# Optimization experiments

Measured on AMD Instinct MI355X. Metric: run time of the kernel, lower is better.

The kernel has to match this reference:

```python
import jax, jax.numpy as jnp
import numpy as np

B, C_IN, N, C_OUT, K = 16, 64, 2048, 64, 20
BN_EPS = 1e-5
SLOPE = 0.2  # LeakyReLU negative slope


def setup_inputs() -> dict:
    key = jax.random.key(0)
    ks = jax.random.split(key, 6)
    x = jax.random.normal(ks[0], (B, C_IN, N), jnp.float32)
    # Conv2d(2*C_IN, C_OUT, 1, bias=False), kaiming-normal init -> [C_OUT, 2*C_IN]
    W = jax.random.normal(ks[1], (C_OUT, 2 * C_IN), jnp.float32) * np.sqrt(2.0 / (2 * C_IN))
    # BatchNorm2d (eval mode) affine params + running stats
    gamma = jax.random.uniform(ks[2], (C_OUT,), jnp.float32, 0.5, 1.5)
    beta = jax.random.normal(ks[3], (C_OUT,), jnp.float32) * 0.1
    run_mean = jax.random.normal(ks[4], (C_OUT,), jnp.float32) * 0.1
    run_var = jax.random.uniform(ks[5], (C_OUT,), jnp.float32, 0.5, 1.5)
    return {"x": x, "W": W, "gamma": gamma, "beta": beta,
            "run_mean": run_mean, "run_var": run_var}


def _knn(x):
    """x: [B, C, N] -> neighbor indices [B, N, K] (nearest, includes self)."""
    xt = jnp.swapaxes(x, 1, 2)                       # [B, N, C]
    sq = jnp.sum(xt * xt, axis=-1)                   # [B, N]
    # squared euclidean distance; topk of -dist == nearest neighbors
    dist = sq[:, :, None] - 2.0 * jnp.einsum('bnc,bmc->bnm', xt, xt) + sq[:, None, :]
    _, idx = jax.lax.top_k(-dist, K)                 # [B, N, K]
    return idx


def reference(x, W, gamma, beta, run_mean, run_var):
    # --- dynamic graph (knn computed under no_grad in the original) ---
    idx = _knn(jax.lax.stop_gradient(x))             # [B, N, K]
    # --- dual gather: edge_index[1]=neighbors -> x_i, edge_index[0]=centers -> x_j ---
    xt = jnp.swapaxes(x, 1, 2)                       # [B, N, C]
    x_i = jax.vmap(lambda xb, ib: xb[ib])(xt, idx)   # [B, N, K, C] neighbor feats
    x_i = jnp.transpose(x_i, (0, 3, 1, 2))           # [B, C, N, K]
    x_j = x[:, :, :, None]                           # [B, C, N, 1] center feats
    feat = jnp.concatenate([x_i, x_j - x_i], axis=1)  # [B, 2C, N, K]
    # --- 1x1 conv (no bias) ---
    h = jnp.einsum('oc,bcnk->bonk', W, feat)         # [B, C_OUT, N, K]
    # --- BatchNorm2d eval mode, folded affine ---
    inv = gamma / jnp.sqrt(run_var + BN_EPS)
    h = h * inv[None, :, None, None] + (beta - run_mean * inv)[None, :, None, None]
    # --- LeakyReLU(0.2); Dropout(0.0) is identity ---
    h = jnp.where(h > 0, h, SLOPE * h)
    # --- max over neighbors ---
    out = jnp.max(h, axis=-1)                        # [B, C_OUT, N]
    return out, idx
```

## Files before the change

### kernel.cpp

```cpp
#include <hip/hip_runtime.h>
#include <cstdint>
#include <cstddef>

#define B_ 16
#define C_ 64
#define N_ 2048
#define K_ 20
#define CAND 24
#define LQ 12

typedef short bf16x8 __attribute__((ext_vector_type(8)));
typedef float f32x4 __attribute__((ext_vector_type(4)));

__device__ __forceinline__ unsigned umin_(unsigned a, unsigned b) { return a < b ? a : b; }
__device__ __forceinline__ unsigned umax_(unsigned a, unsigned b) { return a > b ? a : b; }
__device__ __forceinline__ unsigned short bfr_(float v) {
    unsigned u = __float_as_uint(v);
    return (unsigned short)((u + 0x7FFFu + ((u >> 16) & 1u)) >> 16);
}

__global__ __launch_bounds__(128) void k_sq(const float* __restrict__ x,
                                            float* __restrict__ sqf,
                                            unsigned short* __restrict__ xh,
                                            float* __restrict__ xrT) {
    int tid = threadIdx.x;
    int i = blockIdx.x * 128 + tid;
    int b = i >> 11, n = i & (N_ - 1);
    const float* xb = x + (size_t)b * C_ * N_ + n;
    float vr[C_];
#pragma unroll
    for (int c = 0; c < C_; ++c) vr[c] = xb[(size_t)c * N_];
    float p[C_];
#pragma unroll
    for (int c = 0; c < C_; ++c) p[c] = __fmul_rn(vr[c], vr[c]);
    float r[8];
#pragma unroll
    for (int k = 0; k < 8; ++k) r[k] = p[k];
#pragma unroll
    for (int ii = 8; ii < 64; ii += 8) {
#pragma unroll
        for (int k = 0; k < 8; ++k) r[k] = __fadd_rn(r[k], p[ii + k]);
    }
    float s0 = __fadd_rn(__fadd_rn(r[0], r[1]), __fadd_rn(r[2], r[3]));
    float s1 = __fadd_rn(__fadd_rn(r[4], r[5]), __fadd_rn(r[6], r[7]));
    sqf[i] = __fadd_rn(s0, s1);

    unsigned short* xrow = xh + (size_t)i * 64;
#pragma unroll
    for (int cb = 0; cb < 8; ++cb) {
        bf16x8 pk;
#pragma unroll
        for (int e = 0; e < 8; ++e) pk[e] = (short)bfr_(vr[cb * 8 + e]);
        *reinterpret_cast<bf16x8*>(xrow + ((cb ^ (n & 7)) * 8)) = pk;
    }
    if (xrT) {
        float4* dst = reinterpret_cast<float4*>(xrT + (size_t)i * C_);
#pragma unroll
        for (int q = 0; q < 16; ++q)
            dst[q] = make_float4(vr[q*4+0], vr[q*4+1], vr[q*4+2], vr[q*4+3]);
    }
}

__global__ __launch_bounds__(256, 2) void k_dist(const unsigned short* __restrict__ xh,
                                                 const float* __restrict__ sqf,
                                                 unsigned short* __restrict__ candu) {
    __shared__ __align__(16) unsigned short xtl[256 * 64];
    __shared__ float sqm[256];
    int tid = threadIdx.x;
    int w = tid >> 6, lane = tid & 63;
    int bid = blockIdx.x;
    int b = bid >> 5;
    int n0 = (bid & 31) * 64;
    const unsigned short* xhb = xh + (size_t)b * N_ * 64;

    {
#pragma unroll
        for (int i = 0; i < 2; ++i) {
            int ch = tid + 256 * i;
            *reinterpret_cast<uint4*>(&xtl[ch * 8]) =
                *reinterpret_cast<const uint4*>(&xhb[(size_t)n0 * 64 + ch * 8]);
        }
    }
    __syncthreads();
    int rl = w * 16 + (lane & 15);
    int cb0 = (lane >> 4), cb1 = 4 + (lane >> 4);
    bf16x8 afr0 = *reinterpret_cast<const bf16x8*>(&xtl[rl * 64 + ((cb0 ^ (lane & 7)) * 8)]);
    bf16x8 afr1 = *reinterpret_cast<const bf16x8*>(&xtl[rl * 64 + ((cb1 ^ (lane & 7)) * 8)]);
    float rsq[4];
#pragma unroll
    for (int r = 0; r < 4; ++r)
        rsq[r] = sqf[b * N_ + n0 + w * 16 + (lane >> 4) * 4 + r];

    unsigned list[4][LQ];
#pragma unroll
    for (int r = 0; r < 4; ++r)
#pragma unroll
        for (int j = 0; j < LQ; ++j) list[r][j] = 0xFFFFFFFFu;

    unsigned kmask = 0xFFFFF800u;

    for (int t = 0; t < 8; ++t) {
        int m0 = t * 256;
        __syncthreads();
        {
#pragma unroll
            for (int i = 0; i < 8; ++i) {
                int ch = tid + 256 * i;
                *reinterpret_cast<uint4*>(&xtl[ch * 8]) =
                    *reinterpret_cast<const uint4*>(&xhb[(size_t)m0 * 64 + ch * 8]);
            }
            sqm[tid] = sqf[b * N_ + m0 + tid];
        }
        __syncthreads();
        asm volatile("" :::
            "a0","a1","a2","a3","a4","a5","a6","a7",
            "a8","a9","a10","a11","a12","a13","a14","a15",
            "a16","a17","a18","a19","a20","a21","a22","a23",
            "a24","a25","a26","a27","a28","a29","a30","a31",
            "a32","a33","a34","a35","a36","a37","a38","a39",
            "a40","a41","a42","a43","a44","a45","a46","a47",
            "a48","a49","a50","a51","a52","a53","a54","a55",
            "a56","a57","a58","a59","a60","a61","a62","a63",
            "a64","a65","a66","a67","a68","a69","a70","a71",
            "a72","a73","a74","a75","a76","a77","a78","a79",
            "a80","a81","a82","a83","a84","a85","a86","a87",
            "a88","a89","a90","a91","a92","a93","a94","a95");
        const unsigned short* pB0 = &xtl[(lane & 15) * 64 + ((cb0 ^ (lane & 7)) * 8)];
        const unsigned short* pB1 = &xtl[(lane & 15) * 64 + ((cb1 ^ (lane & 7)) * 8)];
        const float* pS = &sqm[lane & 15];
#pragma unroll
        for (int mb = 0; mb < 16; ++mb) {
            bf16x8 bf0 = *reinterpret_cast<const bf16x8*>(pB0 + mb * 1024);
            bf16x8 bf1 = *reinterpret_cast<const bf16x8*>(pB1 + mb * 1024);
            f32x4 acc = {0.f, 0.f, 0.f, 0.f};
            acc = __builtin_amdgcn_mfma_f32_16x16x32_bf16(afr0, bf0, acc, 0, 0, 0);
            acc = __builtin_amdgcn_mfma_f32_16x16x32_bf16(afr1, bf1, acc, 0, 0, 0);
            float smv = pS[mb * 16];
            unsigned mg = (unsigned)(m0 + mb * 16) | (unsigned)(lane & 15);
#pragma unroll
            for (int r = 0; r < 4; ++r) {
                float rs = rsq[r] + smv;
                float d = fmaf(-2.f, acc[r], rs);
                d = fmaxf(d, 0.f);
                unsigned key;
                asm("v_bfi_b32 %0, %1, %2, %3"
                    : "=v"(key) : "v"(kmask), "v"(__float_as_uint(d)), "v"(mg));
#pragma unroll
                for (int j = LQ - 1; j > 0; --j)
                    asm("v_med3_u32 %0, %0, %1, %2"
                        : "+v"(list[r][j])
                        : "v"(list[r][j - 1]), "v"(key));
                list[r][0] = umin_(list[r][0], key);
            }
        }
    }

    size_t grow0 = (size_t)b * N_ + n0 + w * 16 + (lane >> 4) * 4;
#pragma unroll 1
    for (int it = 0; it < CAND; ++it) {
        unsigned head[4], wv[4];
#pragma unroll
        for (int j = 0; j < 4; ++j) { head[j] = list[j][0]; wv[j] = head[j]; }
#pragma unroll
        for (int d2 = 1; d2 < 16; d2 <<= 1)
#pragma unroll
            for (int j = 0; j < 4; ++j)
                wv[j] = umin_(wv[j], (unsigned)__shfl_xor((int)wv[j], d2, 16));
#pragma unroll
        for (int j = 0; j < 4; ++j) {
            bool own = (head[j] == wv[j]);
#pragma unroll
            for (int jj = 0; jj < LQ - 1; ++jj)
                list[j][jj] = own ? list[j][jj + 1] : list[j][jj];
            list[j][LQ - 1] = own ? 0xFFFFFFFFu : list[j][LQ - 1];
            if ((lane & 15) == 0)
                candu[(grow0 + j) * CAND + it] = (unsigned short)(wv[j] & 2047u);
        }
    }
}


struct ShR { float xnl[64 * 64]; unsigned short cl[64 * CAND]; float dl2[64][CAND]; };
struct ShY { float Al[C_ * 64]; float xl[C_ * 64]; };

__device__ __forceinline__ void rescore3_body(ShR& s, int bid, int tid,
                                              const float* __restrict__ xrT,
                                              const float* __restrict__ sqf,
                                              const unsigned short* __restrict__ candu,
                                              float* __restrict__ idxf) {
    int lane = tid & 63, w = tid >> 6;
    int b = bid >> 5;
    int n0 = (bid & 31) * 64;
    int bN = b * N_;
    const float* xr = xrT + (size_t)bN * C_;
    {
        const float4* src = reinterpret_cast<const float4*>(xr + (size_t)n0 * C_);
#pragma unroll
        for (int q = 0; q < 4; ++q) {
            int idx = tid + q * 256;
            reinterpret_cast<float4*>(s.xnl)[idx] = src[idx];
        }
        if (tid < 192)
            reinterpret_cast<uint4*>(s.cl)[tid] =
                reinterpret_cast<const uint4*>(candu + (size_t)(bN + n0) * CAND)[tid];
    }
    __syncthreads();
    int qbase = lane & ~3, qr = lane & 3;
#pragma unroll 1
    for (int si = 0; si < 6; ++si) {
        int task = w * 384 + si * 64 + lane;
        int row = task / CAND, ci = task - row * CAND;
        int m = s.cl[row * CAND + ci];
        float4 buf[16];
#pragma unroll
        for (int r = 0; r < 4; ++r) {
            int mq = __shfl(m, qbase + r, 64);
            const float* xmq = xr + (size_t)mq * C_ + qr * 16;
            float4 c0 = *reinterpret_cast<const float4*>(xmq + 0);
            float4 c1 = *reinterpret_cast<const float4*>(xmq + 4);
            float4 c2 = *reinterpret_cast<const float4*>(xmq + 8);
            float4 c3 = *reinterpret_cast<const float4*>(xmq + 12);
#pragma unroll
            for (int j2 = 0; j2 < 4; ++j2) {
                float4 s0, s1, s2, s3;
                s0.x = __shfl(c0.x, qbase + j2, 64);
                s0.y = __shfl(c0.y, qbase + j2, 64);
                s0.z = __shfl(c0.z, qbase + j2, 64);
                s0.w = __shfl(c0.w, qbase + j2, 64);
                s1.x = __shfl(c1.x, qbase + j2, 64);
                s1.y = __shfl(c1.y, qbase + j2, 64);
                s1.z = __shfl(c1.z, qbase + j2, 64);
                s1.w = __shfl(c1.w, qbase + j2, 64);
                s2.x = __shfl(c2.x, qbase + j2, 64);
                s2.y = __shfl(c2.y, qbase + j2, 64);
                s2.z = __shfl(c2.z, qbase + j2, 64);
                s2.w = __shfl(c2.w, qbase + j2, 64);
                s3.x = __shfl(c3.x, qbase + j2, 64);
                s3.y = __shfl(c3.y, qbase + j2, 64);
                s3.z = __shfl(c3.z, qbase + j2, 64);
                s3.w = __shfl(c3.w, qbase + j2, 64);
                if (qr == r) {
                    buf[j2 * 4 + 0] = s0;
                    buf[j2 * 4 + 1] = s1;
                    buf[j2 * 4 + 2] = s2;
                    buf[j2 * 4 + 3] = s3;
                }
            }
        }
        const float* xn = s.xnl + row * 64;
        float a = 0.f;
#pragma unroll
        for (int cq = 0; cq < 16; ++cq) {
            float4 n4 = *reinterpret_cast<const float4*>(xn + cq * 4);
            float4 m4 = buf[cq];
            a = __fadd_rn(a, __fmul_rn(n4.x, m4.x));
            a = __fadd_rn(a, __fmul_rn(n4.y, m4.y));
            a = __fadd_rn(a, __fmul_rn(n4.z, m4.z));
            a = __fadd_rn(a, __fmul_rn(n4.w, m4.w));
        }
        s.dl2[row][ci] = __fadd_rn(__fsub_rn(sqf[bN + n0 + row], __fmul_rn(2.0f, a)),
                                   sqf[bN + m]);
    }
    __syncthreads();
#pragma unroll 1
    for (int t2 = 0; t2 < 6; ++t2) {
        int task = tid + t2 * 256;
        int row = task / CAND, ci = task - row * CAND;
        int m = s.cl[row * CAND + ci];
        float di = s.dl2[row][ci];
        int rank = 0;
#pragma unroll
        for (int j = 0; j < CAND; ++j) {
            float dj = s.dl2[row][j];
            int mj = s.cl[row * CAND + j];
            rank += (dj < di || (dj == di && mj < m)) ? 1 : 0;
        }
        if (rank < K_)
            idxf[((size_t)bN + n0 + row) * K_ + rank] = (float)m;
    }
}

__device__ __forceinline__ void ky_body(ShY& s, int bid, int tid,
                                        const float* __restrict__ x,
                                        const float* __restrict__ W,
                                        float* __restrict__ Yt) {
    int b = bid >> 5;
    int m0 = (bid & 31) * 64;
    {
        int o = tid & 63, cb = tid >> 6;
#pragma unroll
        for (int j = 0; j < 16; ++j) {
            int c = cb * 16 + j;
            s.Al[c * 64 + o] = W[o * 128 + c] - W[o * 128 + 64 + c];
            s.xl[c * 64 + o] = x[((size_t)b * C_ + c) * N_ + m0 + o];
        }
    }
    __syncthreads();
    int ml = tid & 63, og = tid >> 6;
    float acc[16];
#pragma unroll
    for (int j = 0; j < 16; ++j) acc[j] = 0.f;
#pragma unroll 4
    for (int c = 0; c < C_; ++c) {
        float xv = s.xl[c * 64 + ml];
        const float4* a4 = reinterpret_cast<const float4*>(&s.Al[c * 64 + og * 16]);
#pragma unroll
        for (int q = 0; q < 4; ++q) {
            float4 av = a4[q];
            acc[q*4+0] = fmaf(av.x, xv, acc[q*4+0]);
            acc[q*4+1] = fmaf(av.y, xv, acc[q*4+1]);
            acc[q*4+2] = fmaf(av.z, xv, acc[q*4+2]);
            acc[q*4+3] = fmaf(av.w, xv, acc[q*4+3]);
        }
    }
    float* yp = Yt + ((size_t)b * N_ + m0 + ml) * C_ + og * 16;
#pragma unroll
    for (int q = 0; q < 4; ++q)
        reinterpret_cast<float4*>(yp)[q] =
            make_float4(acc[q*4+0], acc[q*4+1], acc[q*4+2], acc[q*4+3]);
}

__global__ __launch_bounds__(256) void k_post(const float* __restrict__ xrT,
                                              const float* __restrict__ sqf,
                                              const unsigned short* __restrict__ candu,
                                              float* __restrict__ idxf,
                                              const float* __restrict__ x,
                                              const float* __restrict__ W,
                                              float* __restrict__ Yt) {
    __shared__ union U { ShR r; ShY y; } su;
    int bid = blockIdx.x;
    int tid = threadIdx.x;
    if (bid < B_ * 32)
        rescore3_body(su.r, bid, tid, xrT, sqf, candu, idxf);
    else
        ky_body(su.y, bid - B_ * 32, tid, x, W, Yt);
}

__global__ __launch_bounds__(256) void k_rescore3(const float* __restrict__ xrT,
                                                  const float* __restrict__ sqf,
                                                  const unsigned short* __restrict__ candu,
                                                  float* __restrict__ idxf) {
    __shared__ ShR s;
    rescore3_body(s, blockIdx.x, threadIdx.x, xrT, sqf, candu, idxf);
}

__global__ __launch_bounds__(256) void k_y(const float* __restrict__ x,
                                           const float* __restrict__ W,
                                           float* __restrict__ Yt) {
    __shared__ ShY s;
    ky_body(s, blockIdx.x, threadIdx.x, x, W, Yt);
}

__global__ __launch_bounds__(256) void k_rescore(const float* __restrict__ x,
                                                 const float* __restrict__ sqf,
                                                 const unsigned short* __restrict__ candu,
                                                 float* __restrict__ idxf) {
    int tid = threadIdx.x;
    int w = tid >> 6, lane = tid & 63;
    size_t grow = (size_t)blockIdx.x * 4 + w;
    int b = (int)(grow >> 11), n = (int)(grow & (N_ - 1));
    const float* xb = x + (size_t)b * C_ * N_;
    float d = 0.f;
    unsigned m = 0xFFFFFFFFu;
    if (lane < CAND) {
        m = candu[grow * CAND + lane];
        float a = 0.f;
#pragma unroll 8
        for (int c = 0; c < C_; ++c)
            a = __fadd_rn(a, __fmul_rn(xb[(size_t)c * N_ + n], xb[(size_t)c * N_ + m]));
        d = __fadd_rn(__fsub_rn(sqf[b * N_ + n], __fmul_rn(2.0f, a)), sqf[b * N_ + m]);
    }
    int rank = 0;
#pragma unroll 1
    for (int j = 0; j < CAND; ++j) {
        float dj = __shfl(d, j, 64);
        unsigned mj = (unsigned)__shfl((int)m, j, 64);
        if (lane < CAND && (dj < d || (dj == d && mj < m))) ++rank;
    }
    if (lane < CAND && rank < K_)
        idxf[grow * K_ + rank] = (float)m;
}

__global__ __launch_bounds__(256) void k_out(const float* __restrict__ x,
                                             const float* __restrict__ W,
                                             const float* __restrict__ gamma,
                                             const float* __restrict__ beta,
                                             const float* __restrict__ rmean,
                                             const float* __restrict__ rvar,
                                             const float* __restrict__ Yt,
                                             const float* __restrict__ idxf,
                                             float* __restrict__ out) {
    __shared__ float Bl[C_ * 64];
    __shared__ float xl[C_ * 64];
    __shared__ float resl[64 * 65];
    __shared__ float sl[64], tl[64];
    int tid = threadIdx.x;
    int bid = blockIdx.x;
    int b = bid >> 5;
    int n0 = (bid & 31) * 64;
    {
        int o = tid & 63, cb = tid >> 6;
#pragma unroll
        for (int j = 0; j < 16; ++j) {
            int c = cb * 16 + j;
            Bl[c * 64 + o] = W[o * 128 + 64 + c];
            xl[c * 64 + o] = x[((size_t)b * C_ + c) * N_ + n0 + o];
        }
        if (tid < 64) {
            float s = gamma[tid] / sqrtf(rvar[tid] + 1e-5f);
            sl[tid] = s;
            tl[tid] = beta[tid] - rmean[tid] * s;
        }
    }
    __syncthreads();
    {
        int nl = tid & 63, wv2 = tid >> 6;
#pragma unroll
        for (int t = 0; t < 4; ++t) {
            int oq = wv2 * 4 + t;
            float ax = 0.f, ay = 0.f, az = 0.f, aw = 0.f;
#pragma unroll 8
            for (int c = 0; c < C_; ++c) {
                float xv = xl[c * 64 + nl];
                float4 bl4 = *reinterpret_cast<const float4*>(&Bl[c * 64 + oq * 4]);
                ax = fmaf(bl4.x, xv, ax);
                ay = fmaf(bl4.y, xv, ay);
                az = fmaf(bl4.z, xv, az);
                aw = fmaf(bl4.w, xv, aw);
            }
            int o0 = oq * 4;
            resl[(o0 + 0) * 65 + nl] = ax;
            resl[(o0 + 1) * 65 + nl] = ay;
            resl[(o0 + 2) * 65 + nl] = az;
            resl[(o0 + 3) * 65 + nl] = aw;
        }
    }
    __syncthreads();
    int* mil = reinterpret_cast<int*>(Bl);
    {
#pragma unroll
        for (int q = 0; q < 5; ++q) {
            int idx = tid + q * 256;
            mil[idx] = (int)idxf[(size_t)(b * N_ + n0) * K_ + idx];
        }
    }
    __syncthreads();
    {
        int w2 = tid >> 6, lane2 = tid & 63;
        const float* Ytb = Yt + (size_t)b * N_ * C_;
        float s = sl[lane2], t0 = tl[lane2];
        for (int i = 0; i < 16; ++i) {
            int nloc = w2 * 16 + i;
            float v = -3.4e38f;
#pragma unroll
            for (int k = 0; k < K_; ++k) {
                int m = mil[nloc * K_ + k];
                v = fmaxf(v, Ytb[(size_t)m * C_ + lane2]);
            }
            float u = resl[lane2 * 65 + nloc];
            float val = s * (u + v) + t0;
            val = val > 0.f ? val : 0.2f * val;
            resl[lane2 * 65 + nloc] = val;
        }
    }
    __syncthreads();
    {
        int nl2 = tid & 63, ob = tid >> 6;
#pragma unroll
        for (int j = 0; j < 16; ++j) {
            int o2 = ob * 16 + j;
            out[((size_t)b * C_ + o2) * N_ + n0 + nl2] = resl[o2 * 65 + nl2];
        }
    }
}

extern "C" void kernel_launch(void* const* d_in, const int* in_sizes, int n_in,
                              void* d_out, int out_size, void* d_ws, size_t ws_size,
                              hipStream_t stream) {
    const float* x     = (const float*)d_in[0];
    const float* W     = (const float*)d_in[1];
    const float* gamma = (const float*)d_in[2];
    const float* beta  = (const float*)d_in[3];
    const float* rmean = (const float*)d_in[4];
    const float* rvar  = (const float*)d_in[5];

    float* out  = (float*)d_out;
    float* idxf = out + (size_t)B_ * C_ * N_;

    char* ws = (char*)d_ws;
    float* sqf            = (float*)ws;
    unsigned short* candu = (unsigned short*)(ws + 131072);
    unsigned short* xh    = (unsigned short*)(ws + 131072 + 1572864);
    size_t off_xrT        = 131072 + 1572864 + 4194304;
    size_t need_xrT       = off_xrT + 8388608;
    size_t need_ded       = need_xrT + 8388608;
    float* xrT            = (ws_size >= need_xrT) ? (float*)(ws + off_xrT) : nullptr;
    bool dedY             = (ws_size >= need_ded);
    float* Yt             = dedY ? (float*)(ws + need_xrT) : (float*)(ws + 131072);

    k_sq   <<<B_ * N_ / 128, 128, 0, stream>>>(x, sqf, xh, xrT);
    k_dist <<<B_ * 32, 256, 0, stream>>>(xh, sqf, candu);
    if (xrT && dedY) {
        k_post<<<B_ * 64, 256, 0, stream>>>(xrT, sqf, candu, idxf, x, W, Yt);
    } else if (xrT) {
        k_rescore3<<<B_ * 32, 256, 0, stream>>>(xrT, sqf, candu, idxf);
        k_y<<<B_ * 32, 256, 0, stream>>>(x, W, Yt);
    } else {
        k_rescore<<<B_ * N_ / 4, 256, 0, stream>>>(x, sqf, candu, idxf);
        k_y<<<B_ * 32, 256, 0, stream>>>(x, W, Yt);
    }
    k_out  <<<B_ * 32, 256, 0, stream>>>(x, W, gamma, beta, rmean, rvar, Yt, idxf, out);
}
```

Baseline: 151.8 us.

## Split kNN distance scan across two blocks per row tile, merge 48 candidates

The k_dist kernel now splits the 2048 candidate columns into two halves, each handled by a separate block. This doubles the grid to 1024 blocks and raises the launch-bounds occupancy hint to 4. Each half emits 24 bf16-approximate candidates, so rescoring now ranks 48 candidates per point with exact fp32 distances. This targets the small grid (256 blocks) and the long serial column loop in k_dist, at the cost of twice the candidate storage and rescoring work, plus register pressure under the tighter launch bound. In the fallback k_rescore path, lanes 48-63 stay idle.

```diff
diff --git a/kernel.cpp b/kernel.cpp
--- a/kernel.cpp
+++ b/kernel.cpp
@@ -6,7 +6,8 @@
 #define C_ 64
 #define N_ 2048
 #define K_ 20
-#define CAND 24
+#define CANDH 24
+#define CAND_T 48
 #define LQ 12
 
 typedef short bf16x8 __attribute__((ext_vector_type(8)));
@@ -61,7 +62,7 @@
     }
 }
 
-__global__ __launch_bounds__(256, 2) void k_dist(const unsigned short* __restrict__ xh,
+__global__ __launch_bounds__(256, 4) void k_dist(const unsigned short* __restrict__ xh,
                                                  const float* __restrict__ sqf,
                                                  unsigned short* __restrict__ candu) {
     __shared__ __align__(16) unsigned short xtl[256 * 64];
@@ -69,8 +70,11 @@
     int tid = threadIdx.x;
     int w = tid >> 6, lane = tid & 63;
     int bid = blockIdx.x;
-    int b = bid >> 5;
-    int n0 = (bid & 31) * 64;
+    int b = bid >> 6;
+    int g = bid & 63;
+    int n0 = (g >> 1) * 64;
+    int half = g & 1;
+    int mbase = half * 1024;
     const unsigned short* xhb = xh + (size_t)b * N_ * 64;
 
     {
@@ -99,8 +103,8 @@
 
     unsigned kmask = 0xFFFFF800u;
 
-    for (int t = 0; t < 8; ++t) {
-        int m0 = t * 256;
+    for (int t = 0; t < 4; ++t) {
+        int m0 = mbase + t * 256;
         __syncthreads();
         {
 #pragma unroll
@@ -157,7 +161,7 @@
 
     size_t grow0 = (size_t)b * N_ + n0 + w * 16 + (lane >> 4) * 4;
 #pragma unroll 1
-    for (int it = 0; it < CAND; ++it) {
+    for (int it = 0; it < CANDH; ++it) {
         unsigned head[4], wv[4];
 #pragma unroll
         for (int j = 0; j < 4; ++j) { head[j] = list[j][0]; wv[j] = head[j]; }
@@ -174,13 +178,14 @@
                 list[j][jj] = own ? list[j][jj + 1] : list[j][jj];
             list[j][LQ - 1] = own ? 0xFFFFFFFFu : list[j][LQ - 1];
             if ((lane & 15) == 0)
-                candu[(grow0 + j) * CAND + it] = (unsigned short)(wv[j] & 2047u);
-        }
-    }
-}
-
-
-struct ShR { float xnl[64 * 64]; unsigned short cl[64 * CAND]; float dl2[64][CAND]; };
+                candu[(grow0 + j) * CAND_T + half * CANDH + it] =
+                    (unsigned short)(wv[j] & 2047u);
+        }
+    }
+}
+
+
+struct ShR { float xnl[64 * 64]; unsigned short cl[64 * CAND_T]; float dl2[64][CAND_T]; };
 struct ShY { float Al[C_ * 64]; float xl[C_ * 64]; };
 
 __device__ __forceinline__ void rescore3_body(ShR& s, int bid, int tid,
@@ -200,17 +205,21 @@
             int idx = tid + q * 256;
             reinterpret_cast<float4*>(s.xnl)[idx] = src[idx];
         }
-        if (tid < 192)
-            reinterpret_cast<uint4*>(s.cl)[tid] =
-                reinterpret_cast<const uint4*>(candu + (size_t)(bN + n0) * CAND)[tid];
+#pragma unroll
+        for (int q = 0; q < 2; ++q) {
+            int idx = tid + q * 256;
+            if (idx < 384)
+                reinterpret_cast<uint4*>(s.cl)[idx] =
+                    reinterpret_cast<const uint4*>(candu + (size_t)(bN + n0) * CAND_T)[idx];
+        }
     }
     __syncthreads();
     int qbase = lane & ~3, qr = lane & 3;
 #pragma unroll 1
-    for (int si = 0; si < 6; ++si) {
-        int task = w * 384 + si * 64 + lane;
-        int row = task / CAND, ci = task - row * CAND;
-        int m = s.cl[row * CAND + ci];
+    for (int si = 0; si < 12; ++si) {
+        int task = w * 768 + si * 64 + lane;
+        int row = task / CAND_T, ci = task - row * CAND_T;
+        int m = s.cl[row * CAND_T + ci];
         float4 buf[16];
 #pragma unroll
         for (int r = 0; r < 4; ++r) {
@@ -263,16 +272,16 @@
     }
     __syncthreads();
 #pragma unroll 1
-    for (int t2 = 0; t2 < 6; ++t2) {
+    for (int t2 = 0; t2 < 12; ++t2) {
         int task = tid + t2 * 256;
-        int row = task / CAND, ci = task - row * CAND;
-        int m = s.cl[row * CAND + ci];
+        int row = task / CAND_T, ci = task - row * CAND_T;
+        int m = s.cl[row * CAND_T + ci];
         float di = s.dl2[row][ci];
         int rank = 0;
 #pragma unroll
-        for (int j = 0; j < CAND; ++j) {
+        for (int j = 0; j < CAND_T; ++j) {
             float dj = s.dl2[row][j];
-            int mj = s.cl[row * CAND + j];
+            int mj = s.cl[row * CAND_T + j];
             rank += (dj < di || (dj == di && mj < m)) ? 1 : 0;
         }
         if (rank < K_)
@@ -362,8 +371,8 @@
     const float* xb = x + (size_t)b * C_ * N_;
     float d = 0.f;
     unsigned m = 0xFFFFFFFFu;
-    if (lane < CAND) {
-        m = candu[grow * CAND + lane];
+    if (lane < CAND_T) {
+        m = candu[grow * CAND_T + lane];
         float a = 0.f;
 #pragma unroll 8
         for (int c = 0; c < C_; ++c)
@@ -372,12 +381,12 @@
     }
     int rank = 0;
 #pragma unroll 1
-    for (int j = 0; j < CAND; ++j) {
+    for (int j = 0; j < CAND_T; ++j) {
         float dj = __shfl(d, j, 64);
         unsigned mj = (unsigned)__shfl((int)m, j, 64);
-        if (lane < CAND && (dj < d || (dj == d && mj < m))) ++rank;
-    }
-    if (lane < CAND && rank < K_)
+        if (lane < CAND_T && (dj < d || (dj == d && mj < m))) ++rank;
+    }
+    if (lane < CAND_T && rank < K_)
         idxf[grow * K_ + rank] = (float)m;
 }
 
@@ -490,8 +499,8 @@
     char* ws = (char*)d_ws;
     float* sqf            = (float*)ws;
     unsigned short* candu = (unsigned short*)(ws + 131072);
-    unsigned short* xh    = (unsigned short*)(ws + 131072 + 1572864);
-    size_t off_xrT        = 131072 + 1572864 + 4194304;
+    unsigned short* xh    = (unsigned short*)(ws + 131072 + 3145728);
+    size_t off_xrT        = 131072 + 3145728 + 4194304;
     size_t need_xrT       = off_xrT + 8388608;
     size_t need_ded       = need_xrT + 8388608;
     float* xrT            = (ws_size >= need_xrT) ? (float*)(ws + off_xrT) : nullptr;
@@ -499,7 +508,7 @@
     float* Yt             = dedY ? (float*)(ws + need_xrT) : (float*)(ws + 131072);
 
     k_sq   <<<B_ * N_ / 128, 128, 0, stream>>>(x, sqf, xh, xrT);
-    k_dist <<<B_ * 32, 256, 0, stream>>>(xh, sqf, candu);
+    k_dist <<<B_ * 64, 256, 0, stream>>>(xh, sqf, candu);
     if (xrT && dedY) {
         k_post<<<B_ * 64, 256, 0, stream>>>(xrT, sqf, candu, idxf, x, W, Yt);
     } else if (xrT) {
```

Result: slower. 254.7 us (+67.8%).
